# Optimization experiments

Hardware: AMD Instinct MI355X
Metric: run time of the kernel (lower is better)

## Reference

```python
import jax, jax.numpy as jnp
import numpy as np

N_NODES = 100000
N_EDGES = 3200000
IN_CH = 54
HID = 32        # hidden_channels (concat of 4 heads x 8)
OUT = 64        # out_channels (mean over 4 heads)
HEADS = 4
N_GRAPHS = 512


def _segment_softmax(logits, seg, num_segments):
    # logits: [E, H], seg: [E] target-node index
    m = jax.ops.segment_max(logits, seg, num_segments=num_segments)
    m = jnp.where(jnp.isfinite(m), m, 0.0)
    e = jnp.exp(logits - m[seg])
    s = jax.ops.segment_sum(e, seg, num_segments=num_segments)
    return e / (s[seg] + 1e-16)


def _gatv2(x, src, dst, Wl, bl, Wr, br, att, bias, concat):
    # GATv2Conv (PyG): x_l=lin_l(x), x_r=lin_r(x);
    # e_ij = att . leaky_relu(x_l[j] + x_r[i]); alpha = softmax over incoming edges of i;
    # out_i = sum_j alpha_ij * x_l[j]
    N = x.shape[0]
    H, C = att.shape
    xl = (x @ Wl + bl).reshape(N, H, C)
    xr = (x @ Wr + br).reshape(N, H, C)
    e = jax.nn.leaky_relu(xl[src] + xr[dst], 0.2)       # [E, H, C]
    logits = jnp.einsum('ehc,hc->eh', e, att)            # [E, H]
    alpha = _segment_softmax(logits, dst, N)             # [E, H]
    out = jax.ops.segment_sum(xl[src] * alpha[:, :, None], dst, num_segments=N)  # [N,H,C]
    out = out.reshape(N, H * C) if concat else out.mean(axis=1)
    return out + bias


def setup_inputs() -> dict:
    key = jax.random.key(0)
    ks = jax.random.split(key, 16)
    x = jax.random.normal(ks[0], (N_NODES, IN_CH), dtype=jnp.float32)
    edge_index = jax.random.randint(ks[1], (2, N_EDGES), 0, N_NODES, dtype=jnp.int64 if jax.config.jax_enable_x64 else jnp.int32)
    batch_index = jnp.sort(jax.random.randint(ks[2], (N_NODES,), 0, N_GRAPHS))
    C1 = HID // HEADS  # 8
    s1 = 1.0 / np.sqrt(IN_CH)
    s2 = 1.0 / np.sqrt(HID)
    inp = {
        'x': x, 'edge_index': edge_index, 'batch_index': batch_index,
        # layer 1: GATv2Conv(54 -> 8, heads=4, concat=True)
        'Wl1': jax.random.normal(ks[3], (IN_CH, HEADS * C1)) * s1,
        'bl1': jnp.zeros((HEADS * C1,), jnp.float32),
        'Wr1': jax.random.normal(ks[4], (IN_CH, HEADS * C1)) * s1,
        'br1': jnp.zeros((HEADS * C1,), jnp.float32),
        'att1': jax.random.normal(ks[5], (HEADS, C1)) * (1.0 / np.sqrt(C1)),
        'b1': jnp.zeros((HEADS * C1,), jnp.float32),
        # layer 2: GATv2Conv(32 -> 64, heads=4, concat=False)
        'Wl2': jax.random.normal(ks[6], (HID, HEADS * OUT)) * s2,
        'bl2': jnp.zeros((HEADS * OUT,), jnp.float32),
        'Wr2': jax.random.normal(ks[7], (HID, HEADS * OUT)) * s2,
        'br2': jnp.zeros((HEADS * OUT,), jnp.float32),
        'att2': jax.random.normal(ks[8], (HEADS, OUT)) * (1.0 / np.sqrt(OUT)),
        'b2': jnp.zeros((OUT,), jnp.float32),
    }
    return inp


def reference(x, edge_index, batch_index, Wl1, bl1, Wr1, br1, att1, b1,
              Wl2, bl2, Wr2, br2, att2, b2):
    N = x.shape[0]
    # GATv2Conv adds self-loops by default
    loop = jnp.arange(N, dtype=edge_index.dtype)
    src = jnp.concatenate([edge_index[0], loop])
    dst = jnp.concatenate([edge_index[1], loop])
    h = _gatv2(x, src, dst, Wl1, bl1, Wr1, br1, att1, b1, concat=True)
    h = jax.nn.relu(h)  # BasicGNN inter-layer activation (default 'relu')
    h = _gatv2(h, src, dst, Wl2, bl2, Wr2, br2, att2, b2, concat=False)
    # Mish activation
    h = h * jnp.tanh(jax.nn.softplus(h))
    # global mean pool
    sums = jax.ops.segment_sum(h, batch_index, num_segments=N_GRAPHS)
    cnt = jax.ops.segment_sum(jnp.ones((N,), h.dtype), batch_index, num_segments=N_GRAPHS)
    return sums / jnp.maximum(cnt, 1.0)[:, None]
```

## Files before the change

### kernel.cpp

```cpp
#include <hip/hip_runtime.h>
#include <hip/hip_fp16.h>
#include <cmath>

#define NN 100000
#define NE 3200000
#define ET (NE + NN)
#define IN_CH 54
#define HID 32
#define OUTC 64
#define NG 512

__device__ __forceinline__ float lrelu(float v){ return fmaxf(v, 0.2f*v); }
__device__ __forceinline__ float mishf(float v){
    float sp = (v > 20.f) ? v : log1pf(__expf(v));
    return v * tanhf(sp);
}

__global__ void k_count(const int* __restrict__ ei, int* __restrict__ deg){
    int e = blockIdx.x*blockDim.x + threadIdx.x;
    if (e >= ET) return;
    int dst = (e < NE) ? ei[NE + e] : (e - NE);
    atomicAdd(&deg[dst], 1);
}

__global__ void k_scan_a(const int* __restrict__ deg, int* __restrict__ bsum){
    int i = blockIdx.x*256 + threadIdx.x;
    int v = (i < NN) ? deg[i] : 0;
    __shared__ int ws[4];
    #pragma unroll
    for (int o = 1; o < 64; o <<= 1) v += __shfl_xor(v, o);
    if ((threadIdx.x & 63) == 0) ws[threadIdx.x >> 6] = v;
    __syncthreads();
    if (threadIdx.x == 0) bsum[blockIdx.x] = ws[0] + ws[1] + ws[2] + ws[3];
}

__global__ void k_scan_b(int* __restrict__ bsum, int nb){
    __shared__ int sh[512];
    int t = threadIdx.x;
    int orig = (t < nb) ? bsum[t] : 0;
    sh[t] = orig;
    __syncthreads();
    for (int o = 1; o < 512; o <<= 1){
        int v = (t >= o) ? sh[t-o] : 0;
        __syncthreads();
        sh[t] += v;
        __syncthreads();
    }
    if (t < nb) bsum[t] = sh[t] - orig;
}

__global__ void k_scan_c(const int* __restrict__ deg, const int* __restrict__ boff,
                         int* __restrict__ rp, int* __restrict__ cur){
    int b = blockIdx.x, t = threadIdx.x;
    int i = b*256 + t;
    int v = (i < NN) ? deg[i] : 0;
    __shared__ int sh[256];
    sh[t] = v;
    __syncthreads();
    for (int o = 1; o < 256; o <<= 1){
        int u = (t >= o) ? sh[t-o] : 0;
        __syncthreads();
        sh[t] += u;
        __syncthreads();
    }
    int excl = sh[t] - v + boff[b];
    if (i < NN){ rp[i] = excl; cur[i] = excl; }
    if (i == NN-1) rp[NN] = excl + v;
}

__global__ void k_fill(const int* __restrict__ ei, int* __restrict__ cur, int* __restrict__ col){
    int e = blockIdx.x*blockDim.x + threadIdx.x;
    if (e >= ET) return;
    int src = (e < NE) ? ei[e]      : (e - NE);
    int dst = (e < NE) ? ei[NE + e] : (e - NE);
    int p = atomicAdd(&cur[dst], 1);
    col[p] = src;
}

__global__ void k_gemm1(const float* __restrict__ x,
                        const float* __restrict__ Wl, const float* __restrict__ bl,
                        const float* __restrict__ Wr, const float* __restrict__ br,
                        __half* __restrict__ xl1, __half* __restrict__ xr1){
    int node = (blockIdx.x*blockDim.x + threadIdx.x) >> 6;
    int lane = threadIdx.x & 63;
    if (node >= NN) return;
    int c = lane & 31;
    const float* W = (lane < 32) ? Wl : Wr;
    float acc = (lane < 32) ? bl[c] : br[c];
    const float* xrow = x + (size_t)node * IN_CH;
    #pragma unroll 6
    for (int k = 0; k < IN_CH; ++k)
        acc += xrow[k] * W[k*HID + c];
    __half h = __float2half_rn(acc);
    if (lane < 32) xl1[node*HID + c] = h;
    else           xr1[node*HID + c] = h;
}

__global__ void k_edge1(const __half* __restrict__ xl1, const __half* __restrict__ xr1,
                        const float* __restrict__ att, const float* __restrict__ b1,
                        const int* __restrict__ rp, const int* __restrict__ col,
                        float* __restrict__ hout){
    int node = (blockIdx.x*blockDim.x + threadIdx.x) >> 6;
    int lane = threadIdx.x & 63;
    if (node >= NN) return;
    int cl = lane & 15;
    int slot = lane >> 4;
    float2 xr = __half22float2(*(const __half2*)&xl1[0]);
    xr = __half22float2(*(const __half2*)&xr1[node*HID + 2*cl]);
    float2 at = *(const float2*)&att[2*cl];
    float s = 0.f, acc0 = 0.f, acc1 = 0.f;
    int lo = rp[node], hi = rp[node+1];
    int deg = hi - lo;
    int niter = (deg + 3) >> 2;
    int e0 = lo + slot;

    auto eload = [&](int i)->unsigned{
        int e = e0 + 4*i;
        int ec = min(e, hi-1);
        return *(const unsigned*)&xl1[col[ec]*HID + 2*cl];
    };
    auto eproc = [&](unsigned q, bool valid){
        float2 xlv = __half22float2(__builtin_bit_cast(__half2, q));
        float t0 = xlv.x + xr.x, t1 = xlv.y + xr.y;
        float v0 = lrelu(t0), v1 = lrelu(t1);
        float p = v0*at.x + v1*at.y;
        p += __shfl_xor(p, 1);
        p += __shfl_xor(p, 2);
        float w = valid ? __expf(p) : 0.f;
        s    += w;
        acc0 += w * xlv.x;
        acc1 += w * xlv.y;
    };

    unsigned q0 = eload(0); bool v0 = (e0 < hi);
    unsigned q1 = 0;        bool v1 = false;
    if (niter > 1){ q1 = eload(1); v1 = (e0 + 4 < hi); }
    for (int i = 2; i < niter; ++i){
        unsigned q2 = eload(i); bool v2 = (e0 + 4*i < hi);
        eproc(q0, v0);
        q0 = q1; v0 = v1; q1 = q2; v1 = v2;
    }
    eproc(q0, v0);
    if (niter > 1) eproc(q1, v1);

    acc0 += __shfl_xor(acc0, 16); acc0 += __shfl_xor(acc0, 32);
    acc1 += __shfl_xor(acc1, 16); acc1 += __shfl_xor(acc1, 32);
    s    += __shfl_xor(s,    16); s    += __shfl_xor(s,    32);
    if (slot == 0){
        float inv = 1.f / (s + 1e-16f);
        float2 bb = *(const float2*)&b1[2*cl];
        float2 o;
        o.x = fmaxf(acc0*inv + bb.x, 0.f);
        o.y = fmaxf(acc1*inv + bb.y, 0.f);
        *(float2*)&hout[node*HID + 2*cl] = o;
    }
}

__global__ __launch_bounds__(256) void k_gemm2(const float* __restrict__ h,
                        const float* __restrict__ Wl, const float* __restrict__ bl,
                        __half* __restrict__ xl2){
    __shared__ float WS[HID*256];
    for (int i = threadIdx.x; i < HID*256; i += 256) WS[i] = Wl[i];
    __syncthreads();
    int lane = threadIdx.x & 63, wv = threadIdx.x >> 6;
    float4 b4 = *(const float4*)&bl[4*lane];
    int node0 = blockIdx.x * 32 + wv * 8;
    int nend = min(node0 + 8, NN);
    for (int n = node0; n < nend; ++n){
        const float* hr = h + n*HID;
        float4 a = {0.f,0.f,0.f,0.f};
        #pragma unroll 8
        for (int k = 0; k < HID; ++k){
            float hk = hr[k];
            float4 w = *(const float4*)&WS[k*256 + 4*lane];
            a.x += hk*w.x; a.y += hk*w.y; a.z += hk*w.z; a.w += hk*w.w;
        }
        ushort4 u;
        u.x = __half_as_ushort(__float2half_rn(a.x + b4.x));
        u.y = __half_as_ushort(__float2half_rn(a.y + b4.y));
        u.z = __half_as_ushort(__float2half_rn(a.z + b4.z));
        u.w = __half_as_ushort(__float2half_rn(a.w + b4.w));
        *(ushort4*)&xl2[(size_t)n*256 + 4*lane] = u;
    }
}

__global__ __launch_bounds__(256) void k_edge2(const __half* __restrict__ xl2,
                        const float* __restrict__ h,
                        const float* __restrict__ Wr, const float* __restrict__ br,
                        const float* __restrict__ att, const float* __restrict__ b2,
                        const int* __restrict__ rp, const int* __restrict__ col,
                        const int* __restrict__ batch,
                        float* __restrict__ pool, float* __restrict__ cnt){
    int node = (blockIdx.x*blockDim.x + threadIdx.x) >> 6;
    int lane = threadIdx.x & 63;
    if (node >= NN) return;

    int co = 4*lane;
    float4 xr4 = *(const float4*)&br[co];
    {
        const float* hr = h + node*HID;
        #pragma unroll 8
        for (int k = 0; k < HID; ++k){
            float hk = hr[k];
            float4 w = *(const float4*)&Wr[k*256 + co];
            xr4.x += hk*w.x; xr4.y += hk*w.y; xr4.z += hk*w.z; xr4.w += hk*w.w;
        }
    }
    float4 at4 = *(const float4*)&att[co];
    float s = 0.f;
    float4 acc = {0.f,0.f,0.f,0.f};
    int lo = rp[node], hi = rp[node+1];
    int nb = (hi - lo) >> 2;

    uint2 A0,A1,A2,A3, B0,B1,B2,B3;

#define GLD(P0,P1,P2,P3, e_) do { \
        int s0_ = col[(e_)];   int s1_ = col[(e_)+1]; \
        int s2_ = col[(e_)+2]; int s3_ = col[(e_)+3]; \
        P0 = *(const uint2*)(xl2 + s0_*256 + co); \
        P1 = *(const uint2*)(xl2 + s1_*256 + co); \
        P2 = *(const uint2*)(xl2 + s2_*256 + co); \
        P3 = *(const uint2*)(xl2 + s3_*256 + co); \
    } while(0)

#define PROC1(q) do { \
        float2 f01 = __half22float2(__builtin_bit_cast(__half2, q.x)); \
        float2 f23 = __half22float2(__builtin_bit_cast(__half2, q.y)); \
        float t0 = f01.x + xr4.x, t1 = f01.y + xr4.y; \
        float t2 = f23.x + xr4.z, t3 = f23.y + xr4.w; \
        float v0 = lrelu(t0), v1 = lrelu(t1), v2 = lrelu(t2), v3 = lrelu(t3); \
        float p = v0*at4.x + v1*at4.y + v2*at4.z + v3*at4.w; \
        p += __shfl_xor(p, 1); p += __shfl_xor(p, 2); \
        p += __shfl_xor(p, 4); p += __shfl_xor(p, 8); \
        float w = __expf(p); \
        s += w; \
        acc.x += w*f01.x; acc.y += w*f01.y; acc.z += w*f23.x; acc.w += w*f23.y; \
    } while(0)

#define PROC4(P0,P1,P2,P3) do { PROC1(P0); PROC1(P1); PROC1(P2); PROC1(P3); } while(0)

    int e = lo;
    if (nb > 0){
        GLD(A0,A1,A2,A3, e);
        int b = 1;
        for (; b + 1 < nb; b += 2){
            e += 4; GLD(B0,B1,B2,B3, e);
            PROC4(A0,A1,A2,A3);
            e += 4; GLD(A0,A1,A2,A3, e);
            PROC4(B0,B1,B2,B3);
        }
        if (b < nb){
            e += 4; GLD(B0,B1,B2,B3, e);
            PROC4(A0,A1,A2,A3);
            PROC4(B0,B1,B2,B3);
        } else {
            PROC4(A0,A1,A2,A3);
        }
        e += 4;
    }
    for (; e < hi; ++e){
        int src = col[e];
        uint2 q = *(const uint2*)(xl2 + src*256 + co);
        PROC1(q);
    }
#undef GLD
#undef PROC1
#undef PROC4

    float inv = 1.f / (s + 1e-16f);
    float4 t; t.x = acc.x*inv; t.y = acc.y*inv; t.z = acc.z*inv; t.w = acc.w*inv;
    t.x += __shfl_xor(t.x, 16); t.y += __shfl_xor(t.y, 16);
    t.z += __shfl_xor(t.z, 16); t.w += __shfl_xor(t.w, 16);
    t.x += __shfl_xor(t.x, 32); t.y += __shfl_xor(t.y, 32);
    t.z += __shfl_xor(t.z, 32); t.w += __shfl_xor(t.w, 32);
    if (lane < 16){
        int g = batch[node];
        float4 bb = *(const float4*)&b2[co];
        float o0 = 0.25f*t.x + bb.x;
        float o1 = 0.25f*t.y + bb.y;
        float o2 = 0.25f*t.z + bb.z;
        float o3 = 0.25f*t.w + bb.w;
        float* pg = pool + g*OUTC + co;
        atomicAdd(pg+0, mishf(o0));
        atomicAdd(pg+1, mishf(o1));
        atomicAdd(pg+2, mishf(o2));
        atomicAdd(pg+3, mishf(o3));
        if (lane == 0) atomicAdd(&cnt[g], 1.0f);
    }
}

__global__ void k_pool(const float* __restrict__ pool, const float* __restrict__ cnt,
                       float* __restrict__ out){
    int i = blockIdx.x*blockDim.x + threadIdx.x;
    if (i >= NG*OUTC) return;
    out[i] = pool[i] / fmaxf(cnt[i >> 6], 1.0f);
}

extern "C" void kernel_launch(void* const* d_in, const int* in_sizes, int n_in,
                              void* d_out, int out_size, void* d_ws, size_t ws_size,
                              hipStream_t stream){
    const float* x    = (const float*)d_in[0];
    const int*   ei   = (const int*)  d_in[1];
    const int*   batch= (const int*)  d_in[2];
    const float* Wl1  = (const float*)d_in[3];
    const float* bl1  = (const float*)d_in[4];
    const float* Wr1  = (const float*)d_in[5];
    const float* br1  = (const float*)d_in[6];
    const float* att1 = (const float*)d_in[7];
    const float* b1   = (const float*)d_in[8];
    const float* Wl2  = (const float*)d_in[9];
    const float* bl2  = (const float*)d_in[10];
    const float* Wr2  = (const float*)d_in[11];
    const float* br2  = (const float*)d_in[12];
    const float* att2 = (const float*)d_in[13];
    const float* b2   = (const float*)d_in[14];
    float* out = (float*)d_out;

    char* ws = (char*)d_ws;
    size_t off = 0;
    auto alloc = [&](size_t bytes)->char*{
        char* p = ws + off; off += (bytes + 255) & ~(size_t)255; return p;
    };
    __half* xl1  = (__half*)alloc((size_t)NN*HID*2);
    __half* xr1  = (__half*)alloc((size_t)NN*HID*2);
    float*  hbuf = (float*) alloc((size_t)NN*HID*4);
    __half* xl2  = (__half*)alloc((size_t)NN*256*2);
    int*    deg  = (int*)   alloc((size_t)NN*4);
    int*    rp   = (int*)   alloc((size_t)(NN+1)*4);
    int*    cur  = (int*)   alloc((size_t)NN*4);
    int*    col  = (int*)   alloc((size_t)ET*4);
    float*  pool = (float*) alloc((size_t)NG*OUTC*4);
    float*  cnt  = (float*) alloc((size_t)NG*4);
    int*    bsum = (int*)   alloc((size_t)512*4);

    const int NB = (NN + 255) / 256;

    hipMemsetAsync(deg,  0, (size_t)NN*4,      stream);
    hipMemsetAsync(pool, 0, (size_t)NG*OUTC*4, stream);
    hipMemsetAsync(cnt,  0, (size_t)NG*4,      stream);

    k_count <<<(ET+255)/256, 256, 0, stream>>>(ei, deg);
    k_scan_a<<<NB, 256, 0, stream>>>(deg, bsum);
    k_scan_b<<<1, 512, 0, stream>>>(bsum, NB);
    k_scan_c<<<NB, 256, 0, stream>>>(deg, bsum, rp, cur);
    k_fill  <<<(ET+255)/256, 256, 0, stream>>>(ei, cur, col);
    k_gemm1 <<<(NN+3)/4, 256, 0, stream>>>(x, Wl1, bl1, Wr1, br1, xl1, xr1);
    k_edge1 <<<(NN+3)/4, 256, 0, stream>>>(xl1, xr1, att1, b1, rp, col, hbuf);
    k_gemm2 <<<(NN+31)/32, 256, 0, stream>>>(hbuf, Wl2, bl2, xl2);
    k_edge2 <<<(NN+3)/4, 256, 0, stream>>>(xl2, hbuf, Wr2, br2, att2, b2, rp, col, batch, pool, cnt);
    k_pool  <<<(NG*OUTC+255)/256, 256, 0, stream>>>(pool, cnt, out);
}
```

Baseline: 1.159 ms.

## Process two edges per wavefront in layer-2 edge kernel with wider loads

```diff
diff --git a/kernel.cpp b/kernel.cpp
--- a/kernel.cpp
+++ b/kernel.cpp
@@ -194,99 +194,104 @@
     int node = (blockIdx.x*blockDim.x + threadIdx.x) >> 6;
     int lane = threadIdx.x & 63;
     if (node >= NN) return;
-
-    int co = 4*lane;
-    float4 xr4 = *(const float4*)&br[co];
+    int half = lane >> 5, l32 = lane & 31;
+    int chb  = 8*l32;
+
+    float xr[8], at[8];
     {
+        float4 bb0 = *(const float4*)&br[chb];
+        float4 bb1 = *(const float4*)&br[chb + 4];
+        xr[0]=bb0.x; xr[1]=bb0.y; xr[2]=bb0.z; xr[3]=bb0.w;
+        xr[4]=bb1.x; xr[5]=bb1.y; xr[6]=bb1.z; xr[7]=bb1.w;
         const float* hr = h + node*HID;
         #pragma unroll 8
         for (int k = 0; k < HID; ++k){
             float hk = hr[k];
-            float4 w = *(const float4*)&Wr[k*256 + co];
-            xr4.x += hk*w.x; xr4.y += hk*w.y; xr4.z += hk*w.z; xr4.w += hk*w.w;
+            const float* wrow = Wr + (size_t)k*256 + chb;
+            float4 w0 = *(const float4*)wrow;
+            float4 w1 = *(const float4*)(wrow + 4);
+            xr[0] += hk*w0.x; xr[1] += hk*w0.y; xr[2] += hk*w0.z; xr[3] += hk*w0.w;
+            xr[4] += hk*w1.x; xr[5] += hk*w1.y; xr[6] += hk*w1.z; xr[7] += hk*w1.w;
         }
-    }
-    float4 at4 = *(const float4*)&att[co];
+        float4 t0 = *(const float4*)&att[chb];
+        float4 t1 = *(const float4*)&att[chb + 4];
+        at[0]=t0.x; at[1]=t0.y; at[2]=t0.z; at[3]=t0.w;
+        at[4]=t1.x; at[5]=t1.y; at[6]=t1.z; at[7]=t1.w;
+    }
+
     float s = 0.f;
-    float4 acc = {0.f,0.f,0.f,0.f};
+    float acc[8];
+    #pragma unroll
+    for (int i = 0; i < 8; ++i) acc[i] = 0.f;
+
     int lo = rp[node], hi = rp[node+1];
-    int nb = (hi - lo) >> 2;
-
-    uint2 A0,A1,A2,A3, B0,B1,B2,B3;
-
-#define GLD(P0,P1,P2,P3, e_) do { \
-        int s0_ = col[(e_)];   int s1_ = col[(e_)+1]; \
-        int s2_ = col[(e_)+2]; int s3_ = col[(e_)+3]; \
-        P0 = *(const uint2*)(xl2 + s0_*256 + co); \
-        P1 = *(const uint2*)(xl2 + s1_*256 + co); \
-        P2 = *(const uint2*)(xl2 + s2_*256 + co); \
-        P3 = *(const uint2*)(xl2 + s3_*256 + co); \
+    int deg = hi - lo;
+    int ns   = (deg + 1) >> 1;
+    int ns3  = ((ns + 2)/3)*3;
+
+    uint4 A, B, C;
+
+#define GLD(Q, st_) do { \
+        int ei_  = 2*(st_) + half; \
+        int eic_ = min(ei_, deg-1); \
+        int src_ = col[lo + eic_]; \
+        Q = *(const uint4*)(xl2 + (size_t)src_*256 + chb); \
     } while(0)
 
-#define PROC1(q) do { \
-        float2 f01 = __half22float2(__builtin_bit_cast(__half2, q.x)); \
-        float2 f23 = __half22float2(__builtin_bit_cast(__half2, q.y)); \
-        float t0 = f01.x + xr4.x, t1 = f01.y + xr4.y; \
-        float t2 = f23.x + xr4.z, t3 = f23.y + xr4.w; \
-        float v0 = lrelu(t0), v1 = lrelu(t1), v2 = lrelu(t2), v3 = lrelu(t3); \
-        float p = v0*at4.x + v1*at4.y + v2*at4.z + v3*at4.w; \
-        p += __shfl_xor(p, 1); p += __shfl_xor(p, 2); \
-        p += __shfl_xor(p, 4); p += __shfl_xor(p, 8); \
-        float w = __expf(p); \
-        s += w; \
-        acc.x += w*f01.x; acc.y += w*f01.y; acc.z += w*f23.x; acc.w += w*f23.y; \
+#define PROC(Q, st_) do { \
+        float2 f_; float xlf[8]; \
+        f_ = __half22float2(__builtin_bit_cast(__half2, Q.x)); xlf[0]=f_.x; xlf[1]=f_.y; \
+        f_ = __half22float2(__builtin_bit_cast(__half2, Q.y)); xlf[2]=f_.x; xlf[3]=f_.y; \
+        f_ = __half22float2(__builtin_bit_cast(__half2, Q.z)); xlf[4]=f_.x; xlf[5]=f_.y; \
+        f_ = __half22float2(__builtin_bit_cast(__half2, Q.w)); xlf[6]=f_.x; xlf[7]=f_.y; \
+        float p_ = lrelu(xlf[0]+xr[0])*at[0] + lrelu(xlf[1]+xr[1])*at[1] \
+                 + lrelu(xlf[2]+xr[2])*at[2] + lrelu(xlf[3]+xr[3])*at[3] \
+                 + lrelu(xlf[4]+xr[4])*at[4] + lrelu(xlf[5]+xr[5])*at[5] \
+                 + lrelu(xlf[6]+xr[6])*at[6] + lrelu(xlf[7]+xr[7])*at[7]; \
+        p_ += __shfl_xor(p_, 1); \
+        p_ += __shfl_xor(p_, 2); \
+        p_ += __shfl_xor(p_, 4);       \
+        float w_ = ((2*(st_) + half) < deg) ? __expf(p_) : 0.f; \
+        s += w_; \
+        acc[0] += w_*xlf[0]; acc[1] += w_*xlf[1]; \
+        acc[2] += w_*xlf[2]; acc[3] += w_*xlf[3]; \
+        acc[4] += w_*xlf[4]; acc[5] += w_*xlf[5]; \
+        acc[6] += w_*xlf[6]; acc[7] += w_*xlf[7]; \
     } while(0)
 
-#define PROC4(P0,P1,P2,P3) do { PROC1(P0); PROC1(P1); PROC1(P2); PROC1(P3); } while(0)
-
-    int e = lo;
-    if (nb > 0){
-        GLD(A0,A1,A2,A3, e);
-        int b = 1;
-        for (; b + 1 < nb; b += 2){
-            e += 4; GLD(B0,B1,B2,B3, e);
-            PROC4(A0,A1,A2,A3);
-            e += 4; GLD(A0,A1,A2,A3, e);
-            PROC4(B0,B1,B2,B3);
-        }
-        if (b < nb){
-            e += 4; GLD(B0,B1,B2,B3, e);
-            PROC4(A0,A1,A2,A3);
-            PROC4(B0,B1,B2,B3);
-        } else {
-            PROC4(A0,A1,A2,A3);
-        }
-        e += 4;
-    }
-    for (; e < hi; ++e){
-        int src = col[e];
-        uint2 q = *(const uint2*)(xl2 + src*256 + co);
-        PROC1(q);
-    }
+    GLD(A, 0);
+    GLD(B, 1);
+    GLD(C, 2);
+    for (int st = 3; st < ns3; st += 3){
+        PROC(A, st-3); GLD(A, st);
+        PROC(B, st-2); GLD(B, st+1);
+        PROC(C, st-1); GLD(C, st+2);
+    }
+    PROC(A, ns3-3);
+    PROC(B, ns3-2);
+    PROC(C, ns3-1);
 #undef GLD
-#undef PROC1
-#undef PROC4
-
+#undef PROC
+
+    s += __shfl_xor(s, 32);
     float inv = 1.f / (s + 1e-16f);
-    float4 t; t.x = acc.x*inv; t.y = acc.y*inv; t.z = acc.z*inv; t.w = acc.w*inv;
-    t.x += __shfl_xor(t.x, 16); t.y += __shfl_xor(t.y, 16);
-    t.z += __shfl_xor(t.z, 16); t.w += __shfl_xor(t.w, 16);
-    t.x += __shfl_xor(t.x, 32); t.y += __shfl_xor(t.y, 32);
-    t.z += __shfl_xor(t.z, 32); t.w += __shfl_xor(t.w, 32);
-    if (lane < 16){
-        int g = batch[node];
-        float4 bb = *(const float4*)&b2[co];
-        float o0 = 0.25f*t.x + bb.x;
-        float o1 = 0.25f*t.y + bb.y;
-        float o2 = 0.25f*t.z + bb.z;
-        float o3 = 0.25f*t.w + bb.w;
-        float* pg = pool + g*OUTC + co;
-        atomicAdd(pg+0, mishf(o0));
-        atomicAdd(pg+1, mishf(o1));
-        atomicAdd(pg+2, mishf(o2));
-        atomicAdd(pg+3, mishf(o3));
-        if (lane == 0) atomicAdd(&cnt[g], 1.0f);
-    }
+    #pragma unroll
+    for (int i = 0; i < 8; ++i){
+        float v = acc[i] + __shfl_xor(acc[i], 32);
+        v *= inv;
+        v += __shfl_xor(v, 8);
+        v += __shfl_xor(v, 16);
+        acc[i] = v;
+    }
+    int grp = batch[node];
+    if (half == 0 && l32 < 8){
+        float* pg = pool + grp*OUTC + 8*l32;
+        const float* bb = b2 + 8*l32;
+        #pragma unroll
+        for (int i = 0; i < 8; ++i)
+            atomicAdd(pg + i, mishf(0.25f*acc[i] + bb[i]));
+    }
+    if (lane == 0) atomicAdd(&cnt[grp], 1.0f);
 }
 
 __global__ void k_pool(const float* __restrict__ pool, const float* __restrict__ cnt,
```

New measurement: 1.412 ms. 1.22x slower.
